# Kernel tuning notes

Measured on AMD Instinct MI355X. Metric: run time of the kernel, lower is better.

Reference implementation:

```python
import jax, jax.numpy as jnp
import numpy as np

B, T_TEXT, HID = 16, 512, 512
MAX_LEN = 2048
DP_CH, DP_K = 256, 3
PP_CH, PP_K, PP_LAYERS = 384, 5, 5
N_BINS = 256


def conv1d_same(x, w, b, pad):
    # x: [B, C_in, T], w: [C_out, C_in, K] -> [B, C_out, T]
    xp = jnp.pad(x, ((0, 0), (0, 0), (pad, pad)))
    y = jax.lax.conv_general_dilated(xp, w, (1,), 'VALID',
                                     dimension_numbers=('NCH', 'OIH', 'NCH'))
    return y + b[None, :, None]


def channel_ln(x, g, beta, eps=1e-5):
    # LayerNorm over channel dim of [B, C, T] (torch LayerNorm with dim=1)
    m = jnp.mean(x, axis=1, keepdims=True)
    v = jnp.mean((x - m) ** 2, axis=1, keepdims=True)
    return (x - m) / jnp.sqrt(v + eps) * g[None, :, None] + beta[None, :, None]


def sinusoidal_pos(T, dim):
    # fairseq-style sinusoidal embedding, positions start at padding_idx+1 = 1
    half = dim // 2
    inv = jnp.exp(jnp.arange(half, dtype=jnp.float32) * (-np.log(10000.0) / (half - 1)))
    pos = jnp.arange(1, T + 1, dtype=jnp.float32)
    ang = pos[:, None] * inv[None, :]
    return jnp.concatenate([jnp.sin(ang), jnp.cos(ang)], axis=1)  # [T, dim]


def setup_inputs() -> dict:
    key = jax.random.key(0)
    ks = jax.random.split(key, 16)
    sd = lambda fan: 1.0 / np.sqrt(fan)
    inp = {}
    inp['x'] = jax.random.normal(ks[0], (B, T_TEXT, HID), dtype=jnp.float32)
    inp['duration'] = jax.random.randint(ks[1], (B, T_TEXT), 0, 7, dtype=jnp.int32)
    inp['src_mask'] = jnp.zeros((B, T_TEXT), dtype=bool)
    inp['max_len'] = MAX_LEN
    # duration predictor params (2 conv layers + linear)
    inp['dp_w0'] = jax.random.normal(ks[2], (DP_CH, HID, DP_K)) * sd(HID * DP_K)
    inp['dp_w1'] = jax.random.normal(ks[3], (DP_CH, DP_CH, DP_K)) * sd(DP_CH * DP_K)
    inp['dp_b'] = jnp.zeros((2, DP_CH))
    inp['dp_g'] = jnp.ones((2, DP_CH))
    inp['dp_beta'] = jnp.zeros((2, DP_CH))
    inp['dp_lin_w'] = jax.random.normal(ks[4], (DP_CH, 1)) * sd(DP_CH)
    inp['dp_lin_b'] = jnp.zeros((1,))
    # pitch predictor params (5 conv layers + linear, odim=2 for use_uv)
    inp['pp_w0'] = jax.random.normal(ks[5], (PP_CH, HID, PP_K)) * sd(HID * PP_K)
    inp['pp_w_rest'] = jax.random.normal(ks[6], (PP_LAYERS - 1, PP_CH, PP_CH, PP_K)) * sd(PP_CH * PP_K)
    inp['pp_b'] = jnp.zeros((PP_LAYERS, PP_CH))
    inp['pp_g'] = jnp.ones((PP_LAYERS, PP_CH))
    inp['pp_beta'] = jnp.zeros((PP_LAYERS, PP_CH))
    inp['pp_lin_w'] = jax.random.normal(ks[7], (PP_CH, 2)) * sd(PP_CH)
    inp['pp_lin_b'] = jnp.zeros((2,))
    inp['pos_alpha'] = jnp.ones((1,))
    inp['pitch_emb'] = jax.random.normal(ks[8], (N_BINS, HID)) * 0.02
    inp['pitch_bins'] = jnp.linspace(-1.0, 1.0, N_BINS - 1)  # linear quantization, stats min/max
    return inp


def reference(x, duration, src_mask, max_len, dp_w0, dp_w1, dp_b, dp_g, dp_beta,
              dp_lin_w, dp_lin_b, pp_w0, pp_w_rest, pp_b, pp_g, pp_beta,
              pp_lin_w, pp_lin_b, pos_alpha, pitch_emb, pitch_bins):
    Bn, T, H = x.shape
    keep = 1.0 - src_mask.astype(x.dtype)  # [B,T], 1 where valid

    # ---- DurationPredictor (log-domain durations) ----
    h = jnp.transpose(x, (0, 2, 1))  # [B,H,T]
    for i, w in enumerate([dp_w0, dp_w1]):
        h = conv1d_same(h, w, dp_b[i], (DP_K - 1) // 2)
        h = jax.nn.relu(h)
        h = channel_ln(h, dp_g[i], dp_beta[i])
        h = h * keep[:, None, :]
    log_dur = (jnp.einsum('bct,co->bto', h, dp_lin_w) + dp_lin_b) * keep[:, :, None]
    log_dur = log_dur[..., 0]  # [B,T]

    # ---- LengthRegulator: vectorized variable-repeat via searchsorted ----
    cum = jnp.cumsum(duration, axis=1)  # [B,T]
    frames = jnp.arange(max_len)
    tok = jax.vmap(lambda c: jnp.searchsorted(c, frames, side='right'))(cum)  # [B,max_len]
    mel_len = cum[:, -1]
    fmask = (frames[None, :] < mel_len[:, None]).astype(x.dtype)  # [B,max_len]
    mel = jnp.take_along_axis(x, jnp.minimum(tok, T - 1)[..., None], axis=1) * fmask[..., None]

    # ---- VariancePredictor (pitch, odim=2 for f0 + uv) ----
    pe = sinusoidal_pos(max_len, H)  # [max_len, H]
    p = mel + pos_alpha[0] * pe[None]
    p = jnp.transpose(p, (0, 2, 1))  # [B,H,max_len]
    for i in range(PP_LAYERS):
        w = pp_w0 if i == 0 else pp_w_rest[i - 1]
        p = conv1d_same(p, w, pp_b[i], (PP_K - 1) // 2)
        p = jax.nn.relu(p)
        p = channel_ln(p, pp_g[i], pp_beta[i])
    pitch_pred = jnp.einsum('bct,co->bto', p, pp_lin_w) + pp_lin_b  # [B,max_len,2]

    # ---- bucketize f0 channel + embedding add ----
    idx = jnp.searchsorted(pitch_bins, pitch_pred[..., 0], side='left')  # torch.bucketize
    p_embed = pitch_emb[idx]  # [B,max_len,H]
    out = mel + p_embed
    return out, log_dur, pitch_pred, mel_len
```

## Files before the change

kernel.cpp:

```cpp
#include <hip/hip_runtime.h>
#include <cstdint>
#include <cstddef>

constexpr int BB      = 16;
constexpr int T_TEXT  = 512;
constexpr int HID     = 512;
constexpr int MAX_LEN = 2048;
constexpr int DP_CH   = 256;
constexpr int PP_CH   = 384;

typedef unsigned short u16;
typedef unsigned int   u32;
typedef short bf16x8 __attribute__((ext_vector_type(8)));
typedef float f32x4  __attribute__((ext_vector_type(4)));

__device__ __forceinline__ void gload_lds16(const void* g, void* l) {
  __builtin_amdgcn_global_load_lds(
      (const __attribute__((address_space(1))) u32*)g,
      (__attribute__((address_space(3))) u32*)l, 16, 0, 0);
}

__device__ __forceinline__ u16 f2bf(float v) {
  union { float f; u32 u; } a;
  a.f = v;
  u32 r = (a.u + 0x7FFFu + ((a.u >> 16) & 1u)) >> 16;
  return (u16)r;
}

__global__ __launch_bounds__(256) void pack_w_k(const float* __restrict__ w,
                                                u16* __restrict__ p,
                                                int O, int I, int KT) {
  int NF  = O >> 4, NCB = I >> 5;
  int total = KT * NCB * NF * 64;
  int idx = blockIdx.x * 256 + threadIdx.x;
  if (idx >= total) return;
  int l  = idx & 63;
  int f  = (idx >> 6) % NF;
  int cb = ((idx >> 6) / NF) % NCB;
  int k  = (idx >> 6) / (NF * NCB);
  int o  = f * 16 + (l & 15);
  int ib = cb * 32 + (l >> 4) * 8;
  u16* pd = p + ((size_t)((k * NCB + cb) * NF + f)) * 512 + (size_t)l * 8;
#pragma unroll
  for (int j = 0; j < 8; ++j)
    pd[j] = f2bf(w[((size_t)o * I + ib + j) * KT + k]);
}

template <int CIN, int COUT, int KT, int MT, int WM, int WN, int OPAD, bool F32OUT>
__global__ __launch_bounds__(WM * WN * 64)
void gemm_conv_ln(const u16* __restrict__ a, const u16* __restrict__ wp,
                  const float* __restrict__ bias, const float* __restrict__ gamma,
                  const float* __restrict__ beta,
                  u16* __restrict__ o, float* __restrict__ fo, int T) {
  constexpr int WAVES   = WM * WN;
  constexpr int THREADS = WAVES * 64;
  constexpr int RS    = MT + KT - 1;
  constexpr int NCB   = CIN / 32;
  constexpr int NF    = COUT / 16;
  constexpr int Mfr   = MT / (16 * WM);
  constexpr int Nfr   = NF / WN;
  constexpr int A_ONE = RS * 64;
  constexpr int RED_OFF = 2 * A_ONE;
  static_assert(MT % (16 * WM) == 0 && NF % WN == 0, "tiling");

  const int TpIn  = T + KT - 1;
  const int TpOut = T + 2 * OPAD;

  const int tid  = threadIdx.x;
  const int wave = tid >> 6;
  const int lane = tid & 63;
  const int sl   = lane & 15;
  const int q    = lane >> 4;
  const int wm   = wave / WN;
  const int wn   = wave % WN;
  const int waveM0 = wm * Mfr * 16;
  const int f0   = wn * Nfr;
  const int t0   = blockIdx.x * MT;
  const int b    = blockIdx.y;

  extern __shared__ __align__(16) char smem[];

  const u16* abase_g = a + ((size_t)b * TpIn + t0) * CIN;

  auto stageA = [&](int buf, int cb) {
    char* lbase = smem + buf * A_ONE;
    for (int i = tid; i < RS * 4; i += THREADS) {
      int qc  = i / RS;
      int row = i - qc * RS;
      gload_lds16(abase_g + (size_t)row * CIN + cb * 32 + qc * 8,
                  lbase + (size_t)(i - lane) * 16);
    }
  };
  auto loadB = [&](bf16x8* dst, int k, int cb) {
    const u16* base = wp + ((size_t)(k * NCB + cb) * NF) * 512 + (size_t)lane * 8;
#pragma unroll
    for (int nf = 0; nf < Nfr; ++nf)
      dst[nf] = *(const bf16x8*)(base + (size_t)(f0 + nf) * 512);
  };

  f32x4 acc[Mfr][Nfr];
#pragma unroll
  for (int mf = 0; mf < Mfr; ++mf)
#pragma unroll
    for (int nf = 0; nf < Nfr; ++nf) acc[mf][nf] = (f32x4)0.f;

  bf16x8 Bc[Nfr], Bn[Nfr];
  stageA(0, 0);
  loadB(Bc, 0, 0);
  asm volatile("s_waitcnt vmcnt(0)" ::: "memory");
  __syncthreads();

  int ab = 0;
  for (int cb = 0; cb < NCB; ++cb) {
    if (cb + 1 < NCB) stageA(ab ^ 1, cb + 1);
#pragma unroll
    for (int k = 0; k < KT; ++k) {
      const bool has_next = (k + 1 < KT) || (cb + 1 < NCB);
      if (has_next) {
        int nk  = (k + 1 < KT) ? k + 1 : 0;
        int ncb = (k + 1 < KT) ? cb : cb + 1;
        loadB(Bn, nk, ncb);
      }
      bf16x8 A[Mfr];
      const char* ab_l = smem + ab * A_ONE;
#pragma unroll
      for (int mf = 0; mf < Mfr; ++mf) {
        int row = waveM0 + mf * 16 + sl + k;
        A[mf] = *(const bf16x8*)(ab_l + (q * RS + row) * 16);
      }
#pragma unroll
      for (int nf = 0; nf < Nfr; ++nf)
#pragma unroll
        for (int mf = 0; mf < Mfr; ++mf)
          acc[mf][nf] = __builtin_amdgcn_mfma_f32_16x16x32_bf16(
              A[mf], Bc[nf], acc[mf][nf], 0, 0, 0);
      if (has_next) {
#pragma unroll
        for (int nf = 0; nf < Nfr; ++nf) Bc[nf] = Bn[nf];
      }
    }
    asm volatile("s_waitcnt vmcnt(0)" ::: "memory");
    __syncthreads();
    ab ^= 1;
  }

  float bc[Nfr], gc[Nfr], btc[Nfr];
#pragma unroll
  for (int nf = 0; nf < Nfr; ++nf) {
    int col = (f0 + nf) * 16 + sl;
    bc[nf]  = bias[col];
    gc[nf]  = gamma[col];
    btc[nf] = beta[col];
  }

  float* reds  = (float*)(smem + RED_OFF);
  float* redss = reds + MT * WN;

#pragma unroll
  for (int mf = 0; mf < Mfr; ++mf) {
#pragma unroll
    for (int r = 0; r < 4; ++r) {
      float s = 0.f, ss2 = 0.f;
#pragma unroll
      for (int nf = 0; nf < Nfr; ++nf) {
        float x = acc[mf][nf][r] + bc[nf];
        x = fmaxf(x, 0.f);
        acc[mf][nf][r] = x;
        s += x;
        ss2 = fmaf(x, x, ss2);
      }
#pragma unroll
      for (int off = 1; off < 16; off <<= 1) {
        s   += __shfl_xor(s, off, 64);
        ss2 += __shfl_xor(ss2, off, 64);
      }
      if (sl == 0) {
        int rowb = waveM0 + mf * 16 + q * 4 + r;
        reds[rowb * WN + wn]  = s;
        redss[rowb * WN + wn] = ss2;
      }
    }
  }
  __syncthreads();

#pragma unroll
  for (int mf = 0; mf < Mfr; ++mf) {
#pragma unroll
    for (int r = 0; r < 4; ++r) {
      int rowb = waveM0 + mf * 16 + q * 4 + r;
      float s = 0.f, ss2 = 0.f;
#pragma unroll
      for (int w2 = 0; w2 < WN; ++w2) {
        s   += reds[rowb * WN + w2];
        ss2 += redss[rowb * WN + w2];
      }
      float mean = s * (1.f / COUT);
      float var  = ss2 * (1.f / COUT) - mean * mean;
      float rstd = 1.f / sqrtf(var + 1e-5f);
      int trow = t0 + rowb;
#pragma unroll
      for (int nf = 0; nf < Nfr; ++nf) {
        int col = (f0 + nf) * 16 + sl;
        float y = (acc[mf][nf][r] - mean) * rstd * gc[nf] + btc[nf];
        if constexpr (F32OUT) {
          fo[((size_t)b * T + trow) * COUT + col] = y;
        } else {
          o[((size_t)b * TpOut + OPAD + trow) * COUT + col] = f2bf(y);
        }
      }
    }
  }

  if constexpr (!F32OUT) {
    if (blockIdx.x == 0) {
      for (int i = tid; i < OPAD * COUT; i += THREADS) {
        o[(size_t)b * TpOut * COUT + i] = 0;
        o[((size_t)b * TpOut + OPAD + T) * COUT + i] = 0;
      }
    }
  }
}

constexpr int gemm_lds(int MT, int KT, int WN_) {
  return 2 * (MT + KT - 1) * 64 + MT * WN_ * 8;
}

__global__ __launch_bounds__(256) void split_x_k(const float* __restrict__ x,
                                                 u16* __restrict__ xb) {
  int b = blockIdx.y;
  int row = blockIdx.x * 4 + (threadIdx.x >> 6);
  int lane = threadIdx.x & 63;
  if (row >= T_TEXT + 2) return;
  size_t out = ((size_t)b * (T_TEXT + 2) + row) * HID;
  if (row == 0 || row == T_TEXT + 1) {
    for (int h = lane; h < HID; h += 64) xb[out + h] = 0;
    return;
  }
  const float* xr = x + ((size_t)b * T_TEXT + row - 1) * HID;
  for (int h = lane; h < HID; h += 64) xb[out + h] = f2bf(xr[h]);
}

__global__ __launch_bounds__(256) void dp_head_k(const float* __restrict__ h,
                                                 const float* __restrict__ w,
                                                 const float* __restrict__ b,
                                                 float* __restrict__ out) {
  int tid = threadIdx.x;
  int wv = tid >> 6, lane = tid & 63;
  int row = blockIdx.x * 4 + wv;
  const float* hr = h + (size_t)row * DP_CH;
  float s = 0.f;
  for (int c = lane; c < DP_CH; c += 64) s = fmaf(hr[c], w[c], s);
#pragma unroll
  for (int off = 1; off < 64; off <<= 1) s += __shfl_xor(s, off, 64);
  if (lane == 0) out[row] = s + b[0];
}

__global__ __launch_bounds__(512) void cumsum_k(const int* __restrict__ dur,
                                                int* __restrict__ cum,
                                                float* __restrict__ mel_len_out) {
  __shared__ int s[T_TEXT];
  int b = blockIdx.x, t = threadIdx.x;
  s[t] = dur[b * T_TEXT + t];
  __syncthreads();
  for (int off = 1; off < T_TEXT; off <<= 1) {
    int add = (t >= off) ? s[t - off] : 0;
    __syncthreads();
    s[t] += add;
    __syncthreads();
  }
  cum[b * T_TEXT + t] = s[t];
  if (t == T_TEXT - 1) mel_len_out[b] = (float)s[t];
}

__global__ __launch_bounds__(256) void build_p_k(const float* __restrict__ x,
                                                 const int* __restrict__ cum,
                                                 const float* __restrict__ alpha_p,
                                                 u16* __restrict__ pb) {
  __shared__ int cs[T_TEXT];
  int b = blockIdx.y, tid = threadIdx.x;
  for (int i = tid; i < T_TEXT; i += 256) cs[i] = cum[b * T_TEXT + i];
  __syncthreads();
  int row = blockIdx.x * 4 + (tid >> 6);
  int lane = tid & 63;
  if (row >= MAX_LEN + 4) return;
  size_t out = ((size_t)b * (MAX_LEN + 4) + row) * HID;
  if (row < 2 || row >= MAX_LEN + 2) {
    for (int h = lane; h < HID; h += 64) pb[out + h] = 0;
    return;
  }
  int f = row - 2;
  int lo = 0, hi = T_TEXT;
  while (lo < hi) {
    int mid = (lo + hi) >> 1;
    if (cs[mid] <= f) lo = mid + 1; else hi = mid;
  }
  int src = min(lo, T_TEXT - 1);
  float fm = (f < cs[T_TEXT - 1]) ? 1.f : 0.f;
  float alpha = alpha_p[0];
  const float* xr = x + ((size_t)b * T_TEXT + src) * HID;
  float posf = (float)(f + 1);
  const float kfac = -0.03611898185f;
  for (int h = lane; h < HID / 2; h += 64) {
    float inv = expf((float)h * kfac);
    float ang = posf * inv;
    float sv, cv;
    sincosf(ang, &sv, &cv);
    pb[out + h]           = f2bf(fmaf(alpha, sv, xr[h] * fm));
    pb[out + h + HID / 2] = f2bf(fmaf(alpha, cv, xr[h + HID / 2] * fm));
  }
}

__global__ __launch_bounds__(256) void final_head_k(
    const float* __restrict__ p, const float* __restrict__ x,
    const int* __restrict__ cum, const float* __restrict__ lw,
    const float* __restrict__ lb, const float* __restrict__ bins,
    const float* __restrict__ emb, float* __restrict__ out0,
    float* __restrict__ pred) {
  __shared__ int cs[T_TEXT];
  int b = blockIdx.y, tid = threadIdx.x;
  for (int i = tid; i < T_TEXT; i += 256) cs[i] = cum[b * T_TEXT + i];
  __syncthreads();
  int wv = tid >> 6, lane = tid & 63;
  int f = blockIdx.x * 4 + wv;
  size_t row = (size_t)b * MAX_LEN + f;
  const float* prr = p + row * PP_CH;
  float s0 = 0.f, s1 = 0.f;
  for (int c = lane; c < PP_CH; c += 64) {
    float v = prr[c];
    s0 = fmaf(v, lw[2 * c], s0);
    s1 = fmaf(v, lw[2 * c + 1], s1);
  }
#pragma unroll
  for (int off = 1; off < 64; off <<= 1) {
    s0 += __shfl_xor(s0, off, 64);
    s1 += __shfl_xor(s1, off, 64);
  }
  float p0 = s0 + lb[0];
  float p1 = s1 + lb[1];
  if (lane == 0) {
    pred[row * 2] = p0;
    pred[row * 2 + 1] = p1;
  }
  int lo = 0, hi = 255;
  while (lo < hi) {
    int mid = (lo + hi) >> 1;
    if (bins[mid] < p0) lo = mid + 1; else hi = mid;
  }
  int lo2 = 0, hi2 = T_TEXT;
  while (lo2 < hi2) {
    int mid = (lo2 + hi2) >> 1;
    if (cs[mid] <= f) lo2 = mid + 1; else hi2 = mid;
  }
  int src = min(lo2, T_TEXT - 1);
  float fm = (f < cs[T_TEXT - 1]) ? 1.f : 0.f;
  const float* xr = x + ((size_t)b * T_TEXT + src) * HID;
  const float* er = emb + (size_t)lo * HID;
  float* orow = out0 + row * HID;
  for (int h = lane; h < HID; h += 64) orow[h] = fmaf(xr[h], fm, er[h]);
}

extern "C" void kernel_launch(void* const* d_in, const int* in_sizes, int n_in,
                              void* d_out, int out_size, void* d_ws,
                              size_t ws_size, hipStream_t stream) {
  (void)in_sizes; (void)n_in; (void)out_size; (void)ws_size;

  const float* x          = (const float*)d_in[0];
  const int*   duration   = (const int*)d_in[1];
  const float* dp_w0      = (const float*)d_in[4];
  const float* dp_w1      = (const float*)d_in[5];
  const float* dp_b       = (const float*)d_in[6];
  const float* dp_g       = (const float*)d_in[7];
  const float* dp_beta    = (const float*)d_in[8];
  const float* dp_lin_w   = (const float*)d_in[9];
  const float* dp_lin_b   = (const float*)d_in[10];
  const float* pp_w0      = (const float*)d_in[11];
  const float* pp_w_rest  = (const float*)d_in[12];
  const float* pp_b       = (const float*)d_in[13];
  const float* pp_g       = (const float*)d_in[14];
  const float* pp_beta    = (const float*)d_in[15];
  const float* pp_lin_w   = (const float*)d_in[16];
  const float* pp_lin_b   = (const float*)d_in[17];
  const float* pos_alpha  = (const float*)d_in[18];
  const float* pitch_emb  = (const float*)d_in[19];
  const float* pitch_bins = (const float*)d_in[20];

  char* w8 = (char*)d_ws;
  size_t off = 0;
  auto alloc = [&](size_t bytes) {
    char* pp = w8 + off;
    off += (bytes + 255) & ~(size_t)255;
    return pp;
  };
  u16*   xb    = (u16*)alloc((size_t)BB * 514 * 512 * 2);
  u16*   dp1   = (u16*)alloc((size_t)BB * 514 * 256 * 2);
  float* dp2   = (float*)alloc((size_t)BB * 512 * 256 * 4);
  u16*   Pb    = (u16*)alloc((size_t)BB * 2052 * 512 * 2);
  u16*   ppA   = (u16*)alloc((size_t)BB * 2052 * 384 * 2);
  u16*   ppB   = (u16*)alloc((size_t)BB * 2052 * 384 * 2);
  float* pfin  = (float*)alloc((size_t)BB * 2048 * 384 * 4);
  u16*   pwdp0 = (u16*)alloc((size_t)3 * 512 * 256 * 2);
  u16*   pwdp1 = (u16*)alloc((size_t)3 * 256 * 256 * 2);
  u16*   pwpp0 = (u16*)alloc((size_t)5 * 512 * 384 * 2);
  u16*   pwppr = (u16*)alloc((size_t)4 * 5 * 384 * 384 * 2);
  int*   cum   = (int*)alloc((size_t)BB * T_TEXT * 4);

  float* out0       = (float*)d_out;
  float* log_dur    = out0 + (size_t)BB * MAX_LEN * HID;
  float* pitch_pred = log_dur + (size_t)BB * T_TEXT;
  float* mel_len    = pitch_pred + (size_t)BB * MAX_LEN * 2;

  auto pk = [&](const float* src, u16* dst, int O, int I, int KT) {
    int tot = KT * (I / 32) * (O / 16) * 64;
    pack_w_k<<<dim3((tot + 255) / 256), dim3(256), 0, stream>>>(src, dst, O, I, KT);
  };
  pk(dp_w0, pwdp0, 256, 512, 3);
  pk(dp_w1, pwdp1, 256, 256, 3);
  pk(pp_w0, pwpp0, 384, 512, 5);
  for (int l = 0; l < 4; ++l)
    pk(pp_w_rest + (size_t)l * 384 * 384 * 5,
       pwppr + (size_t)l * (5 * 384 * 384), 384, 384, 5);

  split_x_k<<<dim3(129, BB), dim3(256), 0, stream>>>(x, xb);
  cumsum_k<<<dim3(BB), dim3(512), 0, stream>>>(duration, cum, mel_len);

  constexpr int LDS_DP = gemm_lds(64, 3, 2);
  gemm_conv_ln<512, 256, 3, 64, 2, 2, 1, false>
      <<<dim3(8, BB), dim3(256), LDS_DP, stream>>>(
          xb, pwdp0, dp_b, dp_g, dp_beta, dp1, nullptr, T_TEXT);
  gemm_conv_ln<256, 256, 3, 64, 2, 2, 1, true>
      <<<dim3(8, BB), dim3(256), LDS_DP, stream>>>(
          dp1, pwdp1, dp_b + 256, dp_g + 256, dp_beta + 256,
          nullptr, dp2, T_TEXT);
  dp_head_k<<<dim3(BB * T_TEXT / 4), dim3(256), 0, stream>>>(dp2, dp_lin_w,
                                                             dp_lin_b, log_dur);

  build_p_k<<<dim3(513, BB), dim3(256), 0, stream>>>(x, cum, pos_alpha, Pb);

  constexpr int LDS_PP = gemm_lds(128, 5, 4);
  gemm_conv_ln<512, 384, 5, 128, 2, 4, 2, false>
      <<<dim3(16, BB), dim3(512), LDS_PP, stream>>>(
          Pb, pwpp0, pp_b, pp_g, pp_beta, ppA, nullptr, MAX_LEN);
  gemm_conv_ln<384, 384, 5, 128, 2, 4, 2, false>
      <<<dim3(16, BB), dim3(512), LDS_PP, stream>>>(
          ppA, pwppr + 0 * (5 * 384 * 384),
          pp_b + 384, pp_g + 384, pp_beta + 384, ppB, nullptr, MAX_LEN);
  gemm_conv_ln<384, 384, 5, 128, 2, 4, 2, false>
      <<<dim3(16, BB), dim3(512), LDS_PP, stream>>>(
          ppB, pwppr + 1 * (5 * 384 * 384),
          pp_b + 768, pp_g + 768, pp_beta + 768, ppA, nullptr, MAX_LEN);
  gemm_conv_ln<384, 384, 5, 128, 2, 4, 2, false>
      <<<dim3(16, BB), dim3(512), LDS_PP, stream>>>(
          ppA, pwppr + 2 * (5 * 384 * 384),
          pp_b + 1152, pp_g + 1152, pp_beta + 1152, ppB, nullptr, MAX_LEN);
  gemm_conv_ln<384, 384, 5, 128, 2, 4, 2, true>
      <<<dim3(16, BB), dim3(512), LDS_PP, stream>>>(
          ppB, pwppr + 3 * (5 * 384 * 384),
          pp_b + 1536, pp_g + 1536, pp_beta + 1536, nullptr, pfin, MAX_LEN);

  final_head_k<<<dim3(MAX_LEN / 4, BB), dim3(256), 0, stream>>>(
      pfin, x, cum, pp_lin_w, pp_lin_b, pitch_bins, pitch_emb, out0, pitch_pred);
}
```

Baseline: 505.6 us.

## Stage conv weight tiles through LDS with double buffering instead of register prefetch

Weight (B) fragments were previously loaded directly from global memory into registers, each wave fetching only its own column slice, with a one-step register prefetch. They are now copied cooperatively into a double-buffered LDS region with async global-to-LDS loads, and each wave reads its fragments from LDS. This cuts register pressure and makes the weight loads coalesced block-wide. In exchange it adds a vmcnt wait and a block barrier after every kernel tap instead of once per channel block, and it enlarges the LDS footprint, which may reduce occupancy.

```diff
diff --git a/kernel.cpp b/kernel.cpp
--- a/kernel.cpp
+++ b/kernel.cpp
@@ -60,8 +60,11 @@
   constexpr int Mfr   = MT / (16 * WM);
   constexpr int Nfr   = NF / WN;
   constexpr int A_ONE = RS * 64;
-  constexpr int RED_OFF = 2 * A_ONE;
+  constexpr int B_ONE = NF * 1024;
+  constexpr int B_OFF = 2 * A_ONE;
+  constexpr int RED_OFF = B_OFF + 2 * B_ONE;
   static_assert(MT % (16 * WM) == 0 && NF % WN == 0, "tiling");
+  static_assert((NF * 64) % THREADS == 0, "B chunks split evenly");
 
   const int TpIn  = T + KT - 1;
   const int TpOut = T + 2 * OPAD;
@@ -91,11 +94,12 @@
                   lbase + (size_t)(i - lane) * 16);
     }
   };
-  auto loadB = [&](bf16x8* dst, int k, int cb) {
-    const u16* base = wp + ((size_t)(k * NCB + cb) * NF) * 512 + (size_t)lane * 8;
-#pragma unroll
-    for (int nf = 0; nf < Nfr; ++nf)
-      dst[nf] = *(const bf16x8*)(base + (size_t)(f0 + nf) * 512);
+  auto stageB = [&](int buf, int k, int cb) {
+    const u16* src = wp + ((size_t)(k * NCB + cb) * NF) * 512;
+    char* lbase = smem + B_OFF + buf * B_ONE;
+    for (int i = tid; i < NF * 64; i += THREADS) {
+      gload_lds16(src + (size_t)i * 8, lbase + (size_t)(i - lane) * 16);
+    }
   };
 
   f32x4 acc[Mfr][Nfr];
@@ -104,44 +108,42 @@
 #pragma unroll
     for (int nf = 0; nf < Nfr; ++nf) acc[mf][nf] = (f32x4)0.f;
 
-  bf16x8 Bc[Nfr], Bn[Nfr];
   stageA(0, 0);
-  loadB(Bc, 0, 0);
+  stageB(0, 0, 0);
   asm volatile("s_waitcnt vmcnt(0)" ::: "memory");
   __syncthreads();
 
-  int ab = 0;
+  int ab = 0, bb = 0;
   for (int cb = 0; cb < NCB; ++cb) {
-    if (cb + 1 < NCB) stageA(ab ^ 1, cb + 1);
-#pragma unroll
     for (int k = 0; k < KT; ++k) {
-      const bool has_next = (k + 1 < KT) || (cb + 1 < NCB);
-      if (has_next) {
-        int nk  = (k + 1 < KT) ? k + 1 : 0;
-        int ncb = (k + 1 < KT) ? cb : cb + 1;
-        loadB(Bn, nk, ncb);
-      }
-      bf16x8 A[Mfr];
+      if (k + 1 < KT) {
+        stageB(bb ^ 1, k + 1, cb);
+      } else if (cb + 1 < NCB) {
+        stageB(bb ^ 1, 0, cb + 1);
+        stageA(ab ^ 1, cb + 1);
+      }
+      bf16x8 A[Mfr], Bf[Nfr];
       const char* ab_l = smem + ab * A_ONE;
 #pragma unroll
       for (int mf = 0; mf < Mfr; ++mf) {
         int row = waveM0 + mf * 16 + sl + k;
         A[mf] = *(const bf16x8*)(ab_l + (q * RS + row) * 16);
       }
+      const char* bb_l = smem + B_OFF + bb * B_ONE;
+#pragma unroll
+      for (int nf = 0; nf < Nfr; ++nf)
+        Bf[nf] = *(const bf16x8*)(bb_l + (size_t)(f0 + nf) * 1024 + lane * 16);
 #pragma unroll
       for (int nf = 0; nf < Nfr; ++nf)
 #pragma unroll
         for (int mf = 0; mf < Mfr; ++mf)
           acc[mf][nf] = __builtin_amdgcn_mfma_f32_16x16x32_bf16(
-              A[mf], Bc[nf], acc[mf][nf], 0, 0, 0);
-      if (has_next) {
-#pragma unroll
-        for (int nf = 0; nf < Nfr; ++nf) Bc[nf] = Bn[nf];
-      }
-    }
-    asm volatile("s_waitcnt vmcnt(0)" ::: "memory");
-    __syncthreads();
-    ab ^= 1;
+              A[mf], Bf[nf], acc[mf][nf], 0, 0, 0);
+      asm volatile("s_waitcnt vmcnt(0)" ::: "memory");
+      __syncthreads();
+      bb ^= 1;
+      if (k == KT - 1) ab ^= 1;
+    }
   }
 
   float bc[Nfr], gc[Nfr], btc[Nfr];
@@ -221,8 +223,8 @@
   }
 }
 
-constexpr int gemm_lds(int MT, int KT, int WN_) {
-  return 2 * (MT + KT - 1) * 64 + MT * WN_ * 8;
+constexpr int gemm_lds(int MT, int KT, int COUT, int WN_) {
+  return 2 * (MT + KT - 1) * 64 + 2 * (COUT / 16) * 1024 + MT * WN_ * 8;
 }
 
 __global__ __launch_bounds__(256) void split_x_k(const float* __restrict__ x,
@@ -423,7 +425,7 @@
   split_x_k<<<dim3(129, BB), dim3(256), 0, stream>>>(x, xb);
   cumsum_k<<<dim3(BB), dim3(512), 0, stream>>>(duration, cum, mel_len);
 
-  constexpr int LDS_DP = gemm_lds(64, 3, 2);
+  constexpr int LDS_DP = gemm_lds(64, 3, 256, 2);
   gemm_conv_ln<512, 256, 3, 64, 2, 2, 1, false>
       <<<dim3(8, BB), dim3(256), LDS_DP, stream>>>(
           xb, pwdp0, dp_b, dp_g, dp_beta, dp1, nullptr, T_TEXT);
@@ -436,7 +438,7 @@
 
   build_p_k<<<dim3(513, BB), dim3(256), 0, stream>>>(x, cum, pos_alpha, Pb);
 
-  constexpr int LDS_PP = gemm_lds(128, 5, 4);
+  constexpr int LDS_PP = gemm_lds(128, 5, 384, 4);
   gemm_conv_ln<512, 384, 5, 128, 2, 4, 2, false>
       <<<dim3(16, BB), dim3(512), LDS_PP, stream>>>(
           Pb, pwpp0, pp_b, pp_g, pp_beta, ppA, nullptr, MAX_LEN);
```

After: 443.6 us. 1.14x faster.
